# Kernel tuning notes

Measured on AMD Instinct MI355X. Metric: run time of the kernel, lower is better.

Reference implementation:

```python
import jax, jax.numpy as jnp
import numpy as np

DIM = 2048
INTER = 1408
N_EXPERTS = 16
TOP_K = 2
N_SHARED = 2
SHARED_INTER = N_SHARED * INTER  # 2816


def setup_inputs() -> dict:
    key = jax.random.key(0)
    ks = jax.random.split(key, 9)
    s = 0.02
    return {
        "x": jax.random.normal(ks[0], (4, 2048, DIM), dtype=jnp.float32),
        "gate_w": jax.random.normal(ks[1], (N_EXPERTS, DIM), dtype=jnp.float32) * s,
        "w1": jax.random.normal(ks[2], (N_EXPERTS, INTER, DIM), dtype=jnp.float32) * s,
        "w2": jax.random.normal(ks[3], (N_EXPERTS, DIM, INTER), dtype=jnp.float32) * s,
        "w3": jax.random.normal(ks[4], (N_EXPERTS, INTER, DIM), dtype=jnp.float32) * s,
        "sw1": jax.random.normal(ks[5], (SHARED_INTER, DIM), dtype=jnp.float32) * s,
        "sw2": jax.random.normal(ks[6], (DIM, SHARED_INTER), dtype=jnp.float32) * s,
        "sw3": jax.random.normal(ks[7], (SHARED_INTER, DIM), dtype=jnp.float32) * s,
    }


def _swiglu(t, wa, wb, wo):
    # t: [T, d_in]; wa, wb: [d_h, d_in]; wo: [d_out, d_h]
    h = jax.nn.silu(t @ wa.T) * (t @ wb.T)
    return h @ wo.T


def reference(x, gate_w, w1, w2, w3, sw1, sw2, sw3):
    shape = x.shape
    t = x.reshape(-1, DIM)                      # [T, dim]
    scores = jax.nn.softmax(t @ gate_w.T, axis=-1)  # [T, E]
    weights, indices = jax.lax.top_k(scores, TOP_K)  # [T, k] each

    y = jnp.zeros_like(t)
    # Small fixed loop over experts (structurally distinct weights).
    # Per-token combine weight for expert e: sum over top-k slots routed to e
    # (matches y[idx] += expert(x[idx]) * weights[idx, top]; zero weight for
    # unrouted tokens reproduces the counts[i]==0 skip exactly).
    for e in range(N_EXPERTS):
        w_e = jnp.sum(jnp.where(indices == e, weights, 0.0), axis=-1)  # [T]
        y = y + _swiglu(t, w1[e], w3[e], w2[e]) * w_e[:, None]

    z = _swiglu(t, sw1, sw3, sw2)               # shared experts MLP
    return (y + z).reshape(shape)
```

## Files before the change

### kernel.cpp

```cpp
#include <hip/hip_runtime.h>
#include <hip/hip_bf16.h>

#define DIM 2048
#define INTER 1408
#define NEXP 16
#define NTOK 8192
#define SINTER 2816
#define BM 256
#define BN 128
#define BK 32

typedef __attribute__((ext_vector_type(8))) short bf16x8;
typedef __attribute__((ext_vector_type(4))) float f32x4;
typedef __attribute__((ext_vector_type(8))) unsigned short u16x8;

__device__ __forceinline__ unsigned short f2bf(float f) {
    union { float f; unsigned u; } a; a.f = f;
    unsigned r = a.u + 0x7fffu + ((a.u >> 16) & 1u);
    return (unsigned short)(r >> 16);
}

__device__ __forceinline__ void gload16(const void* g, void* lds) {
    __builtin_amdgcn_global_load_lds(
        (const __attribute__((address_space(1))) void*)g,
        (__attribute__((address_space(3))) void*)lds, 16, 0, 0);
}

__device__ __forceinline__ void stage_f32(const float* g, unsigned short* ldsdst) {
    float4 a = *(const float4*)g;
    float4 b = *(const float4*)(g + 4);
    u16x8 o = { f2bf(a.x), f2bf(a.y), f2bf(a.z), f2bf(a.w),
                f2bf(b.x), f2bf(b.y), f2bf(b.z), f2bf(b.w) };
    *(u16x8*)ldsdst = o;
}

__global__ __launch_bounds__(256) void cast_bf16(const float* __restrict__ s,
                                                 unsigned short* __restrict__ d,
                                                 long long n) {
    long long i = ((long long)blockIdx.x * 256 + threadIdx.x) * 8;
    if (i >= n) return;
    float4 a = *(const float4*)(s + i), b = *(const float4*)(s + i + 4);
    u16x8 o = { f2bf(a.x), f2bf(a.y), f2bf(a.z), f2bf(a.w),
                f2bf(b.x), f2bf(b.y), f2bf(b.z), f2bf(b.w) };
    *(u16x8*)(d + i) = o;
}

__global__ __launch_bounds__(256) void gate_topk(
    const float* __restrict__ x, const float* __restrict__ gw,
    int* __restrict__ counts, int* __restrict__ toklist, float* __restrict__ tokw) {
    int wave = threadIdx.x >> 6;
    int lane = threadIdx.x & 63;
    int tok  = blockIdx.x * 4 + wave;
    const float* xr = x + (size_t)tok * DIM;

    float part[NEXP];
#pragma unroll
    for (int e = 0; e < NEXP; ++e) part[e] = 0.f;
#pragma unroll
    for (int c = 0; c < DIM / 256; ++c) {
        float4 xv = *(const float4*)(xr + c * 256 + lane * 4);
#pragma unroll
        for (int e = 0; e < NEXP; ++e) {
            float4 g = *(const float4*)(gw + e * DIM + c * 256 + lane * 4);
            part[e] += xv.x * g.x + xv.y * g.y + xv.z * g.z + xv.w * g.w;
        }
    }
#pragma unroll
    for (int e = 0; e < NEXP; ++e) {
        float v = part[e];
#pragma unroll
        for (int off = 32; off; off >>= 1) v += __shfl_xor(v, off);
        part[e] = v;
    }
    float mx = part[0];
#pragma unroll
    for (int e = 1; e < NEXP; ++e) mx = fmaxf(mx, part[e]);
    float Z = 0.f;
#pragma unroll
    for (int e = 0; e < NEXP; ++e) Z += expf(part[e] - mx);
    int i1 = 0; float m1 = part[0];
#pragma unroll
    for (int e = 1; e < NEXP; ++e) if (part[e] > m1) { m1 = part[e]; i1 = e; }
    int i2 = -1; float m2 = -1e30f;
#pragma unroll
    for (int e = 0; e < NEXP; ++e) if (e != i1 && part[e] > m2) { m2 = part[e]; i2 = e; }
    if (lane == 0) {
        float w1v = expf(m1 - mx) / Z;
        float w2v = expf(m2 - mx) / Z;
        int p1 = atomicAdd(&counts[i1], 1);
        toklist[i1 * NTOK + p1] = tok; tokw[i1 * NTOK + p1] = w1v;
        int p2 = atomicAdd(&counts[i2], 1);
        toklist[i2 * NTOK + p2] = tok; tokw[i2 * NTOK + p2] = w2v;
    }
}

__global__ void prefix_k(const int* __restrict__ counts, int* __restrict__ base) {
    if (threadIdx.x == 0) {
        int acc = 0;
        for (int e = 0; e < NEXP; ++e) { base[e] = acc; acc += counts[e]; }
        base[16] = acc;
        base[17] = acc + NTOK;
    }
}

template<bool XBF, bool WBF>
__global__ __launch_bounds__(512) void gemm1(
    const float* __restrict__ xf, const unsigned short* __restrict__ xb,
    const float* __restrict__ w1f, const float* __restrict__ w3f,
    const float* __restrict__ sw1f, const float* __restrict__ sw3f,
    const unsigned short* __restrict__ w1b, const unsigned short* __restrict__ w3b,
    const unsigned short* __restrict__ sw1b, const unsigned short* __restrict__ sw3b,
    const int* __restrict__ counts, const int* __restrict__ base,
    const int* __restrict__ toklist, unsigned short* __restrict__ hbuf) {
    const int e   = blockIdx.z;
    const int cnt = (e < NEXP) ? counts[e] : NTOK;
    const int m0  = blockIdx.y * BM;
    if (m0 >= cnt) return;
    const int n0  = blockIdx.x * BN;
    const size_t woff = (size_t)((e < NEXP) ? e : e - NEXP) * INTER * DIM;
    const int hbase = base[e];
    const int* tl = toklist + e * NTOK;

    __shared__ __attribute__((aligned(16))) unsigned short As[BM * BK];
    __shared__ __attribute__((aligned(16))) unsigned short B1s[BN * BK];
    __shared__ __attribute__((aligned(16))) unsigned short B3s[BN * BK];

    const int tid = threadIdx.x;
    const int w = tid >> 6, l = tid & 63;
    const int srow = l >> 2;
    const int scol = (l & 3) * 8;

    int tokA[2];
#pragma unroll
    for (int j = 0; j < 2; ++j) {
        int row  = 32 * w + 16 * j + srow;
        int grow = m0 + row;
        int t;
        if (e >= NEXP) t = grow;
        else t = (grow < cnt) ? tl[grow] : 0;
        tokA[j] = t;
    }
    const int brow = n0 + 16 * w + srow;

    const unsigned short *gA0 = nullptr, *gA1 = nullptr, *gB1 = nullptr, *gB3 = nullptr;
    const float *gA0f = nullptr, *gA1f = nullptr, *gB1f = nullptr, *gB3f = nullptr;
    if constexpr (XBF) {
        gA0 = xb + (size_t)tokA[0] * DIM + scol;
        gA1 = xb + (size_t)tokA[1] * DIM + scol;
    } else {
        gA0f = xf + (size_t)tokA[0] * DIM + scol;
        gA1f = xf + (size_t)tokA[1] * DIM + scol;
    }
    if constexpr (WBF) {
        const unsigned short* b1 = ((e < NEXP) ? w1b : sw1b) + woff;
        const unsigned short* b3 = ((e < NEXP) ? w3b : sw3b) + woff;
        gB1 = b1 + (size_t)brow * DIM + scol;
        gB3 = b3 + (size_t)brow * DIM + scol;
    } else {
        const float* b1 = ((e < NEXP) ? w1f : sw1f) + woff;
        const float* b3 = ((e < NEXP) ? w3f : sw3f) + woff;
        gB1f = b1 + (size_t)brow * DIM + scol;
        gB3f = b3 + (size_t)brow * DIM + scol;
    }

    unsigned short* dA0 = As  + (size_t)(2 * w)     * 512;
    unsigned short* dA1 = As  + (size_t)(2 * w + 1) * 512;
    unsigned short* dB1 = B1s + (size_t)w * 512;
    unsigned short* dB3 = B3s + (size_t)w * 512;

    f32x4 acc1[4][4], acc3[4][4];
#pragma unroll
    for (int m = 0; m < 4; ++m)
#pragma unroll
        for (int n = 0; n < 4; ++n) {
            acc1[m][n] = (f32x4){0.f, 0.f, 0.f, 0.f};
            acc3[m][n] = (f32x4){0.f, 0.f, 0.f, 0.f};
        }

    const int wr = w >> 1, wc = w & 1;
    const int lr = l & 15, lk = (l >> 4) * 8;

    for (int k0 = 0; k0 < DIM; k0 += BK) {
        if constexpr (XBF) {
            gload16(gA0 + k0, dA0);
            gload16(gA1 + k0, dA1);
        } else {
            stage_f32(gA0f + k0, dA0 + l * 8);
            stage_f32(gA1f + k0, dA1 + l * 8);
        }
        if constexpr (WBF) {
            gload16(gB1 + k0, dB1);
            gload16(gB3 + k0, dB3);
        } else {
            stage_f32(gB1f + k0, dB1 + l * 8);
            stage_f32(gB3f + k0, dB3 + l * 8);
        }
        __syncthreads();
        bf16x8 af[4], b1q[4], b3q[4];
#pragma unroll
        for (int m = 0; m < 4; ++m)
            af[m] = *(const bf16x8*)(As + (wr * 64 + m * 16 + lr) * BK + lk);
#pragma unroll
        for (int n = 0; n < 4; ++n) {
            b1q[n] = *(const bf16x8*)(B1s + (wc * 64 + n * 16 + lr) * BK + lk);
            b3q[n] = *(const bf16x8*)(B3s + (wc * 64 + n * 16 + lr) * BK + lk);
        }
#pragma unroll
        for (int m = 0; m < 4; ++m)
#pragma unroll
            for (int n = 0; n < 4; ++n) {
                acc1[m][n] = __builtin_amdgcn_mfma_f32_16x16x32_bf16(af[m], b1q[n], acc1[m][n], 0, 0, 0);
                acc3[m][n] = __builtin_amdgcn_mfma_f32_16x16x32_bf16(af[m], b3q[n], acc3[m][n], 0, 0, 0);
            }
        __syncthreads();
    }
#pragma unroll
    for (int m = 0; m < 4; ++m) {
#pragma unroll
        for (int i = 0; i < 4; ++i) {
            int row  = wr * 64 + m * 16 + (l >> 4) * 4 + i;
            int grow = m0 + row;
            if (grow < cnt) {
                size_t ro = (size_t)(hbase + grow) * INTER;
#pragma unroll
                for (int n = 0; n < 4; ++n) {
                    int col = n0 + wc * 64 + n * 16 + lr;
                    float a = acc1[m][n][i];
                    float h = a / (1.f + __expf(-a)) * acc3[m][n][i];
                    hbuf[ro + col] = f2bf(h);
                }
            }
        }
    }
}

template<bool WBF>
__global__ __launch_bounds__(512) void gemm2(
    const unsigned short* __restrict__ hbuf,
    const float* __restrict__ w2f, const float* __restrict__ sw2f,
    const unsigned short* __restrict__ w2b, const unsigned short* __restrict__ sw2b,
    const int* __restrict__ counts, const int* __restrict__ base,
    const int* __restrict__ toklist, const float* __restrict__ tokw,
    float* __restrict__ out) {
    const int e   = blockIdx.z;
    const int cnt = (e < NEXP) ? counts[e] : NTOK;
    const int m0  = blockIdx.y * BM;
    if (m0 >= cnt) return;
    const int n0  = blockIdx.x * BN;
    const int hbase = base[e];
    const size_t bstride = (e < NEXP) ? INTER : SINTER;

    const unsigned short* Bb = nullptr; const float* Bf = nullptr;
    if constexpr (WBF)
        Bb = (e < NEXP) ? w2b + (size_t)e * DIM * INTER : sw2b + (size_t)(e - NEXP) * INTER;
    else
        Bf = (e < NEXP) ? w2f + (size_t)e * DIM * INTER : sw2f + (size_t)(e - NEXP) * INTER;

    __shared__ __attribute__((aligned(16))) unsigned short As[BM * BK];
    __shared__ __attribute__((aligned(16))) unsigned short Bs[BN * BK];

    const int tid = threadIdx.x;
    const int w = tid >> 6, l = tid & 63;
    const int srow = l >> 2;
    const int scol = (l & 3) * 8;

    const unsigned short* gA0 = hbuf + (size_t)(hbase + m0 + 32 * w + srow) * INTER + scol;
    const unsigned short* gA1 = hbuf + (size_t)(hbase + m0 + 32 * w + 16 + srow) * INTER + scol;
    const int brow = n0 + 16 * w + srow;
    const unsigned short* gB = nullptr; const float* gBf = nullptr;
    if constexpr (WBF) gB  = Bb + (size_t)brow * bstride + scol;
    else               gBf = Bf + (size_t)brow * bstride + scol;

    unsigned short* dA0 = As + (size_t)(2 * w)     * 512;
    unsigned short* dA1 = As + (size_t)(2 * w + 1) * 512;
    unsigned short* dB  = Bs + (size_t)w * 512;

    f32x4 acc[4][4];
#pragma unroll
    for (int m = 0; m < 4; ++m)
#pragma unroll
        for (int n = 0; n < 4; ++n) acc[m][n] = (f32x4){0.f, 0.f, 0.f, 0.f};

    const int wr = w >> 1, wc = w & 1;
    const int lr = l & 15, lk = (l >> 4) * 8;

    for (int k0 = 0; k0 < INTER; k0 += BK) {
        gload16(gA0 + k0, dA0);
        gload16(gA1 + k0, dA1);
        if constexpr (WBF) gload16(gB + k0, dB);
        else               stage_f32(gBf + k0, dB + l * 8);
        __syncthreads();
        bf16x8 af[4], bq[4];
#pragma unroll
        for (int m = 0; m < 4; ++m)
            af[m] = *(const bf16x8*)(As + (wr * 64 + m * 16 + lr) * BK + lk);
#pragma unroll
        for (int n = 0; n < 4; ++n)
            bq[n] = *(const bf16x8*)(Bs + (wc * 64 + n * 16 + lr) * BK + lk);
#pragma unroll
        for (int m = 0; m < 4; ++m)
#pragma unroll
            for (int n = 0; n < 4; ++n)
                acc[m][n] = __builtin_amdgcn_mfma_f32_16x16x32_bf16(af[m], bq[n], acc[m][n], 0, 0, 0);
        __syncthreads();
    }
#pragma unroll
    for (int m = 0; m < 4; ++m) {
#pragma unroll
        for (int i = 0; i < 4; ++i) {
            int row  = wr * 64 + m * 16 + (l >> 4) * 4 + i;
            int grow = m0 + row;
            if (grow < cnt) {
                int tok; float wt;
                if (e < NEXP) { tok = toklist[e * NTOK + grow]; wt = tokw[e * NTOK + grow]; }
                else          { tok = grow; wt = 1.f; }
                float* orow = out + (size_t)tok * DIM + n0 + wc * 64 + lr;
#pragma unroll
                for (int n = 0; n < 4; ++n)
                    unsafeAtomicAdd(orow + n * 16, acc[m][n][i] * wt);
            }
        }
    }
}

extern "C" void kernel_launch(void* const* d_in, const int* in_sizes, int n_in,
                              void* d_out, int out_size, void* d_ws, size_t ws_size,
                              hipStream_t stream) {
    const float* x   = (const float*)d_in[0];
    const float* gw  = (const float*)d_in[1];
    const float* w1  = (const float*)d_in[2];
    const float* w2  = (const float*)d_in[3];
    const float* w3  = (const float*)d_in[4];
    const float* sw1 = (const float*)d_in[5];
    const float* sw2 = (const float*)d_in[6];
    const float* sw3 = (const float*)d_in[7];
    float* out = (float*)d_out;

    char* ws = (char*)d_ws;
    int*   counts  = (int*)ws;
    int*   basep   = (int*)(ws + 128);
    int*   toklist = (int*)(ws + 4096);
    float* tokw    = (float*)(ws + 4096 + (size_t)NEXP * NTOK * 4);
    unsigned short* hbuf = (unsigned short*)(ws + (2u << 20));

    const size_t hbytes = (size_t)4 * NTOK * INTER * 2;
    const size_t offx   = (2ull << 20) + hbytes;
    const size_t xbytes = (size_t)NTOK * DIM * 2;
    const size_t offw   = offx + xbytes;
    const size_t wB     = (size_t)NEXP * INTER * DIM * 2;
    const size_t swB    = (size_t)SINTER * DIM * 2;
    const size_t tier2_end = offw + 3 * wB + 3 * swB;

    int tier = (ws_size >= tier2_end) ? 2 : (ws_size >= offw ? 1 : 0);

    unsigned short* xb   = (unsigned short*)(ws + offx);
    unsigned short* w1b  = (unsigned short*)(ws + offw);
    unsigned short* w3b  = (unsigned short*)(ws + offw + wB);
    unsigned short* w2b  = (unsigned short*)(ws + offw + 2 * wB);
    unsigned short* sw1b = (unsigned short*)(ws + offw + 3 * wB);
    unsigned short* sw3b = (unsigned short*)(ws + offw + 3 * wB + swB);
    unsigned short* sw2b = (unsigned short*)(ws + offw + 3 * wB + 2 * swB);

    hipMemsetAsync(counts, 0, 64, stream);
    hipMemsetAsync(d_out, 0, (size_t)out_size * sizeof(float), stream);

    gate_topk<<<NTOK / 4, 256, 0, stream>>>(x, gw, counts, toklist, tokw);
    prefix_k<<<1, 64, 0, stream>>>(counts, basep);

    auto cast = [&](const float* s, unsigned short* d, long long n) {
        cast_bf16<<<(int)((n / 8 + 255) / 256), 256, 0, stream>>>(s, d, n);
    };
    if (tier >= 1) cast(x, xb, (long long)NTOK * DIM);
    if (tier == 2) {
        cast(w1, w1b, (long long)NEXP * INTER * DIM);
        cast(w3, w3b, (long long)NEXP * INTER * DIM);
        cast(w2, w2b, (long long)NEXP * INTER * DIM);
        cast(sw1, sw1b, (long long)SINTER * DIM);
        cast(sw3, sw3b, (long long)SINTER * DIM);
        cast(sw2, sw2b, (long long)SINTER * DIM);
    }

    dim3 g1(INTER / BN, NTOK / BM, 18);
    dim3 g2(DIM / BN, NTOK / BM, 18);
    if (tier == 2) {
        gemm1<true, true><<<g1, 512, 0, stream>>>(x, xb, w1, w3, sw1, sw3,
            w1b, w3b, sw1b, sw3b, counts, basep, toklist, hbuf);
        gemm2<true><<<g2, 512, 0, stream>>>(hbuf, w2, sw2, w2b, sw2b,
            counts, basep, toklist, tokw, out);
    } else if (tier == 1) {
        gemm1<true, false><<<g1, 512, 0, stream>>>(x, xb, w1, w3, sw1, sw3,
            w1b, w3b, sw1b, sw3b, counts, basep, toklist, hbuf);
        gemm2<false><<<g2, 512, 0, stream>>>(hbuf, w2, sw2, w2b, sw2b,
            counts, basep, toklist, tokw, out);
    } else {
        gemm1<false, false><<<g1, 512, 0, stream>>>(x, xb, w1, w3, sw1, sw3,
            w1b, w3b, sw1b, sw3b, counts, basep, toklist, hbuf);
        gemm2<false><<<g2, 512, 0, stream>>>(hbuf, w2, sw2, w2b, sw2b,
            counts, basep, toklist, tokw, out);
    }
}
```

Baseline: 1.443 ms.

## Add 4-stage LDS prefetch pipeline with swizzled layout and larger gemm2 tile

Both GEMMs now keep four LDS stages and prefetch three K-steps ahead, using explicit vmcnt waits and s_barrier in place of a full __syncthreads after each load. The LDS tiles use an XOR swizzle to reduce bank conflicts, MFMA sections run at raised wave priority, and gemm2's N tile doubles to 256 with each warp covering 8x4 fragments. The fp32 fallback tiers are removed, so the workspace is assumed large enough for the bf16 weight copies. The aim is to hide global-load latency and sync stalls, at the cost of much more LDS (occupancy is capped at two blocks) and more registers in gemm2.

```diff
diff --git a/kernel.cpp b/kernel.cpp
--- a/kernel.cpp
+++ b/kernel.cpp
@@ -6,9 +6,6 @@
 #define NEXP 16
 #define NTOK 8192
 #define SINTER 2816
-#define BM 256
-#define BN 128
-#define BK 32
 
 typedef __attribute__((ext_vector_type(8))) short bf16x8;
 typedef __attribute__((ext_vector_type(4))) float f32x4;
@@ -24,14 +21,6 @@
     __builtin_amdgcn_global_load_lds(
         (const __attribute__((address_space(1))) void*)g,
         (__attribute__((address_space(3))) void*)lds, 16, 0, 0);
-}
-
-__device__ __forceinline__ void stage_f32(const float* g, unsigned short* ldsdst) {
-    float4 a = *(const float4*)g;
-    float4 b = *(const float4*)(g + 4);
-    u16x8 o = { f2bf(a.x), f2bf(a.y), f2bf(a.z), f2bf(a.w),
-                f2bf(b.x), f2bf(b.y), f2bf(b.z), f2bf(b.w) };
-    *(u16x8*)ldsdst = o;
 }
 
 __global__ __launch_bounds__(256) void cast_bf16(const float* __restrict__ s,
@@ -103,70 +92,56 @@
     }
 }
 
-template<bool XBF, bool WBF>
-__global__ __launch_bounds__(512) void gemm1(
-    const float* __restrict__ xf, const unsigned short* __restrict__ xb,
-    const float* __restrict__ w1f, const float* __restrict__ w3f,
-    const float* __restrict__ sw1f, const float* __restrict__ sw3f,
+__device__ __forceinline__ int swz(int r) { return (r ^ (r >> 2)) & 3; }
+
+__global__ __launch_bounds__(512, 2) void gemm1(
+    const unsigned short* __restrict__ xb,
     const unsigned short* __restrict__ w1b, const unsigned short* __restrict__ w3b,
     const unsigned short* __restrict__ sw1b, const unsigned short* __restrict__ sw3b,
     const int* __restrict__ counts, const int* __restrict__ base,
     const int* __restrict__ toklist, unsigned short* __restrict__ hbuf) {
     const int e   = blockIdx.z;
     const int cnt = (e < NEXP) ? counts[e] : NTOK;
-    const int m0  = blockIdx.y * BM;
+    const int m0  = blockIdx.y * 256;
     if (m0 >= cnt) return;
-    const int n0  = blockIdx.x * BN;
+    const int n0  = blockIdx.x * 128;
     const size_t woff = (size_t)((e < NEXP) ? e : e - NEXP) * INTER * DIM;
+    const unsigned short* B1 = ((e < NEXP) ? w1b : sw1b) + woff;
+    const unsigned short* B3 = ((e < NEXP) ? w3b : sw3b) + woff;
     const int hbase = base[e];
     const int* tl = toklist + e * NTOK;
 
-    __shared__ __attribute__((aligned(16))) unsigned short As[BM * BK];
-    __shared__ __attribute__((aligned(16))) unsigned short B1s[BN * BK];
-    __shared__ __attribute__((aligned(16))) unsigned short B3s[BN * BK];
+    __shared__ __attribute__((aligned(16))) unsigned short As[4][8192];
+    __shared__ __attribute__((aligned(16))) unsigned short B1s[4][4096];
+    __shared__ __attribute__((aligned(16))) unsigned short B3s[4][4096];
 
     const int tid = threadIdx.x;
     const int w = tid >> 6, l = tid & 63;
-    const int srow = l >> 2;
-    const int scol = (l & 3) * 8;
-
-    int tokA[2];
-#pragma unroll
-    for (int j = 0; j < 2; ++j) {
-        int row  = 32 * w + 16 * j + srow;
-        int grow = m0 + row;
-        int t;
-        if (e >= NEXP) t = grow;
-        else t = (grow < cnt) ? tl[grow] : 0;
-        tokA[j] = t;
-    }
-    const int brow = n0 + 16 * w + srow;
-
-    const unsigned short *gA0 = nullptr, *gA1 = nullptr, *gB1 = nullptr, *gB3 = nullptr;
-    const float *gA0f = nullptr, *gA1f = nullptr, *gB1f = nullptr, *gB3f = nullptr;
-    if constexpr (XBF) {
-        gA0 = xb + (size_t)tokA[0] * DIM + scol;
-        gA1 = xb + (size_t)tokA[1] * DIM + scol;
-    } else {
-        gA0f = xf + (size_t)tokA[0] * DIM + scol;
-        gA1f = xf + (size_t)tokA[1] * DIM + scol;
-    }
-    if constexpr (WBF) {
-        const unsigned short* b1 = ((e < NEXP) ? w1b : sw1b) + woff;
-        const unsigned short* b3 = ((e < NEXP) ? w3b : sw3b) + woff;
-        gB1 = b1 + (size_t)brow * DIM + scol;
-        gB3 = b3 + (size_t)brow * DIM + scol;
-    } else {
-        const float* b1 = ((e < NEXP) ? w1f : sw1f) + woff;
-        const float* b3 = ((e < NEXP) ? w3f : sw3f) + woff;
-        gB1f = b1 + (size_t)brow * DIM + scol;
-        gB3f = b3 + (size_t)brow * DIM + scol;
-    }
-
-    unsigned short* dA0 = As  + (size_t)(2 * w)     * 512;
-    unsigned short* dA1 = As  + (size_t)(2 * w + 1) * 512;
-    unsigned short* dB1 = B1s + (size_t)w * 512;
-    unsigned short* dB3 = B3s + (size_t)w * 512;
+    const int wr = w >> 1, wc = w & 1;
+    const int lr = l & 15, hi = l >> 4;
+
+    const int row0 = tid >> 2, row1 = row0 + 128;
+    const int c0 = (tid & 3) ^ swz(row0);
+    int g0 = m0 + row0, g1 = m0 + row1;
+    int t0, t1;
+    if (e < NEXP) { t0 = (g0 < cnt) ? tl[g0] : 0; t1 = (g1 < cnt) ? tl[g1] : 0; }
+    else          { t0 = g0; t1 = g1; }
+    const unsigned short* aSrc0 = xb + (size_t)t0 * DIM + c0 * 8;
+    const unsigned short* aSrc1 = xb + (size_t)t1 * DIM + c0 * 8;
+    const unsigned short* b1Src = B1 + (size_t)(n0 + row0) * DIM + c0 * 8;
+    const unsigned short* b3Src = B3 + (size_t)(n0 + row0) * DIM + c0 * 8;
+
+    int aoff[4], boff[4];
+#pragma unroll
+    for (int m = 0; m < 4; ++m) {
+        int r = wr * 64 + m * 16 + lr;
+        aoff[m] = r * 64 + ((swz(r) ^ hi) << 4);
+    }
+#pragma unroll
+    for (int n = 0; n < 4; ++n) {
+        int r = wc * 64 + n * 16 + lr;
+        boff[n] = r * 64 + ((swz(r) ^ hi) << 4);
+    }
 
     f32x4 acc1[4][4], acc3[4][4];
 #pragma unroll
@@ -177,48 +152,60 @@
             acc3[m][n] = (f32x4){0.f, 0.f, 0.f, 0.f};
         }
 
-    const int wr = w >> 1, wc = w & 1;
-    const int lr = l & 15, lk = (l >> 4) * 8;
-
-    for (int k0 = 0; k0 < DIM; k0 += BK) {
-        if constexpr (XBF) {
-            gload16(gA0 + k0, dA0);
-            gload16(gA1 + k0, dA1);
-        } else {
-            stage_f32(gA0f + k0, dA0 + l * 8);
-            stage_f32(gA1f + k0, dA1 + l * 8);
-        }
-        if constexpr (WBF) {
-            gload16(gB1 + k0, dB1);
-            gload16(gB3 + k0, dB3);
-        } else {
-            stage_f32(gB1f + k0, dB1 + l * 8);
-            stage_f32(gB3f + k0, dB3 + l * 8);
-        }
-        __syncthreads();
-        bf16x8 af[4], b1q[4], b3q[4];
+    const int H = DIM / 32;
+
+    auto STAGE = [&](int hh) {
+        int hb = hh & 3;
+        int kc = hh * 32;
+        gload16(aSrc0 + kc, &As[hb][tid * 8]);
+        gload16(aSrc1 + kc, &As[hb][4096 + tid * 8]);
+        gload16(b1Src + kc, &B1s[hb][tid * 8]);
+        gload16(b3Src + kc, &B3s[hb][tid * 8]);
+    };
+
+    STAGE(0); STAGE(1); STAGE(2);
+    asm volatile("s_waitcnt vmcnt(8)" ::: "memory");
+    __builtin_amdgcn_s_barrier();
+
+    for (int h = 0; h < H; ++h) {
+        const int hb = h & 3;
+        bf16x8 af[4], b1f[4], b3f[4];
 #pragma unroll
         for (int m = 0; m < 4; ++m)
-            af[m] = *(const bf16x8*)(As + (wr * 64 + m * 16 + lr) * BK + lk);
+            af[m] = *(const bf16x8*)((const char*)&As[hb][0] + aoff[m]);
 #pragma unroll
         for (int n = 0; n < 4; ++n) {
-            b1q[n] = *(const bf16x8*)(B1s + (wc * 64 + n * 16 + lr) * BK + lk);
-            b3q[n] = *(const bf16x8*)(B3s + (wc * 64 + n * 16 + lr) * BK + lk);
-        }
+            b1f[n] = *(const bf16x8*)((const char*)&B1s[hb][0] + boff[n]);
+            b3f[n] = *(const bf16x8*)((const char*)&B3s[hb][0] + boff[n]);
+        }
+        if (h + 3 < H) {
+            STAGE(h + 3);
+            asm volatile("s_waitcnt vmcnt(8)" ::: "memory");
+        } else if (h == H - 3) {
+            asm volatile("s_waitcnt vmcnt(4)" ::: "memory");
+        } else if (h == H - 2) {
+            asm volatile("s_waitcnt vmcnt(0)" ::: "memory");
+        }
+        __builtin_amdgcn_s_barrier();
+        asm volatile("s_waitcnt lgkmcnt(0)" ::: "memory");
+        __builtin_amdgcn_sched_barrier(0);
+        __builtin_amdgcn_s_setprio(1);
 #pragma unroll
         for (int m = 0; m < 4; ++m)
 #pragma unroll
             for (int n = 0; n < 4; ++n) {
-                acc1[m][n] = __builtin_amdgcn_mfma_f32_16x16x32_bf16(af[m], b1q[n], acc1[m][n], 0, 0, 0);
-                acc3[m][n] = __builtin_amdgcn_mfma_f32_16x16x32_bf16(af[m], b3q[n], acc3[m][n], 0, 0, 0);
+                acc1[m][n] = __builtin_amdgcn_mfma_f32_16x16x32_bf16(af[m], b1f[n], acc1[m][n], 0, 0, 0);
+                acc3[m][n] = __builtin_amdgcn_mfma_f32_16x16x32_bf16(af[m], b3f[n], acc3[m][n], 0, 0, 0);
             }
-        __syncthreads();
-    }
+        __builtin_amdgcn_s_setprio(0);
+        __builtin_amdgcn_s_barrier();
+    }
+
 #pragma unroll
     for (int m = 0; m < 4; ++m) {
 #pragma unroll
         for (int i = 0; i < 4; ++i) {
-            int row  = wr * 64 + m * 16 + (l >> 4) * 4 + i;
+            int row  = wr * 64 + m * 16 + hi * 4 + i;
             int grow = m0 + row;
             if (grow < cnt) {
                 size_t ro = (size_t)(hbase + grow) * INTER;
@@ -226,89 +213,113 @@
                 for (int n = 0; n < 4; ++n) {
                     int col = n0 + wc * 64 + n * 16 + lr;
                     float a = acc1[m][n][i];
-                    float h = a / (1.f + __expf(-a)) * acc3[m][n][i];
-                    hbuf[ro + col] = f2bf(h);
+                    float hv = a / (1.f + __expf(-a)) * acc3[m][n][i];
+                    hbuf[ro + col] = f2bf(hv);
                 }
             }
         }
     }
 }
 
-template<bool WBF>
-__global__ __launch_bounds__(512) void gemm2(
+__global__ __launch_bounds__(512, 2) void gemm2(
     const unsigned short* __restrict__ hbuf,
-    const float* __restrict__ w2f, const float* __restrict__ sw2f,
     const unsigned short* __restrict__ w2b, const unsigned short* __restrict__ sw2b,
     const int* __restrict__ counts, const int* __restrict__ base,
     const int* __restrict__ toklist, const float* __restrict__ tokw,
     float* __restrict__ out) {
     const int e   = blockIdx.z;
     const int cnt = (e < NEXP) ? counts[e] : NTOK;
-    const int m0  = blockIdx.y * BM;
+    const int m0  = blockIdx.y * 256;
     if (m0 >= cnt) return;
-    const int n0  = blockIdx.x * BN;
+    const int n0  = blockIdx.x * 256;
     const int hbase = base[e];
     const size_t bstride = (e < NEXP) ? INTER : SINTER;
-
-    const unsigned short* Bb = nullptr; const float* Bf = nullptr;
-    if constexpr (WBF)
-        Bb = (e < NEXP) ? w2b + (size_t)e * DIM * INTER : sw2b + (size_t)(e - NEXP) * INTER;
-    else
-        Bf = (e < NEXP) ? w2f + (size_t)e * DIM * INTER : sw2f + (size_t)(e - NEXP) * INTER;
-
-    __shared__ __attribute__((aligned(16))) unsigned short As[BM * BK];
-    __shared__ __attribute__((aligned(16))) unsigned short Bs[BN * BK];
+    const unsigned short* Bb = (e < NEXP) ? w2b + (size_t)e * DIM * INTER
+                                          : sw2b + (size_t)(e - NEXP) * INTER;
+
+    __shared__ __attribute__((aligned(16))) unsigned short Ah[4][8192];
+    __shared__ __attribute__((aligned(16))) unsigned short Bh[4][8192];
 
     const int tid = threadIdx.x;
     const int w = tid >> 6, l = tid & 63;
-    const int srow = l >> 2;
-    const int scol = (l & 3) * 8;
-
-    const unsigned short* gA0 = hbuf + (size_t)(hbase + m0 + 32 * w + srow) * INTER + scol;
-    const unsigned short* gA1 = hbuf + (size_t)(hbase + m0 + 32 * w + 16 + srow) * INTER + scol;
-    const int brow = n0 + 16 * w + srow;
-    const unsigned short* gB = nullptr; const float* gBf = nullptr;
-    if constexpr (WBF) gB  = Bb + (size_t)brow * bstride + scol;
-    else               gBf = Bf + (size_t)brow * bstride + scol;
-
-    unsigned short* dA0 = As + (size_t)(2 * w)     * 512;
-    unsigned short* dA1 = As + (size_t)(2 * w + 1) * 512;
-    unsigned short* dB  = Bs + (size_t)w * 512;
-
-    f32x4 acc[4][4];
-#pragma unroll
-    for (int m = 0; m < 4; ++m)
+    const int wr = w >> 2, wc = w & 3;
+    const int lr = l & 15, hi = l >> 4;
+
+    const int row0 = tid >> 2, row1 = row0 + 128;
+    const int c0 = (tid & 3) ^ swz(row0);
+    const unsigned short* aSrc0 = hbuf + (size_t)(hbase + m0 + row0) * INTER + c0 * 8;
+    const unsigned short* aSrc1 = hbuf + (size_t)(hbase + m0 + row1) * INTER + c0 * 8;
+    const unsigned short* bSrc0 = Bb + (size_t)(n0 + row0) * bstride + c0 * 8;
+    const unsigned short* bSrc1 = Bb + (size_t)(n0 + row1) * bstride + c0 * 8;
+
+    int aoff[8], boff[4];
+#pragma unroll
+    for (int m = 0; m < 8; ++m) {
+        int r = wr * 128 + m * 16 + lr;
+        aoff[m] = r * 64 + ((swz(r) ^ hi) << 4);
+    }
+#pragma unroll
+    for (int n = 0; n < 4; ++n) {
+        int r = wc * 64 + n * 16 + lr;
+        boff[n] = r * 64 + ((swz(r) ^ hi) << 4);
+    }
+
+    f32x4 acc[8][4];
+#pragma unroll
+    for (int m = 0; m < 8; ++m)
 #pragma unroll
         for (int n = 0; n < 4; ++n) acc[m][n] = (f32x4){0.f, 0.f, 0.f, 0.f};
 
-    const int wr = w >> 1, wc = w & 1;
-    const int lr = l & 15, lk = (l >> 4) * 8;
-
-    for (int k0 = 0; k0 < INTER; k0 += BK) {
-        gload16(gA0 + k0, dA0);
-        gload16(gA1 + k0, dA1);
-        if constexpr (WBF) gload16(gB + k0, dB);
-        else               stage_f32(gBf + k0, dB + l * 8);
-        __syncthreads();
-        bf16x8 af[4], bq[4];
-#pragma unroll
-        for (int m = 0; m < 4; ++m)
-            af[m] = *(const bf16x8*)(As + (wr * 64 + m * 16 + lr) * BK + lk);
+    const int H = INTER / 32;
+
+    auto STAGE = [&](int hh) {
+        int hb = hh & 3;
+        int kc = hh * 32;
+        gload16(aSrc0 + kc, &Ah[hb][tid * 8]);
+        gload16(aSrc1 + kc, &Ah[hb][4096 + tid * 8]);
+        gload16(bSrc0 + kc, &Bh[hb][tid * 8]);
+        gload16(bSrc1 + kc, &Bh[hb][4096 + tid * 8]);
+    };
+
+    STAGE(0); STAGE(1); STAGE(2);
+    asm volatile("s_waitcnt vmcnt(8)" ::: "memory");
+    __builtin_amdgcn_s_barrier();
+
+    for (int h = 0; h < H; ++h) {
+        const int hb = h & 3;
+        bf16x8 af[8], bf[4];
+#pragma unroll
+        for (int m = 0; m < 8; ++m)
+            af[m] = *(const bf16x8*)((const char*)&Ah[hb][0] + aoff[m]);
 #pragma unroll
         for (int n = 0; n < 4; ++n)
-            bq[n] = *(const bf16x8*)(Bs + (wc * 64 + n * 16 + lr) * BK + lk);
-#pragma unroll
-        for (int m = 0; m < 4; ++m)
+            bf[n] = *(const bf16x8*)((const char*)&Bh[hb][0] + boff[n]);
+        if (h + 3 < H) {
+            STAGE(h + 3);
+            asm volatile("s_waitcnt vmcnt(8)" ::: "memory");
+        } else if (h == H - 3) {
+            asm volatile("s_waitcnt vmcnt(4)" ::: "memory");
+        } else if (h == H - 2) {
+            asm volatile("s_waitcnt vmcnt(0)" ::: "memory");
+        }
+        __builtin_amdgcn_s_barrier();
+        asm volatile("s_waitcnt lgkmcnt(0)" ::: "memory");
+        __builtin_amdgcn_sched_barrier(0);
+        __builtin_amdgcn_s_setprio(1);
+#pragma unroll
+        for (int m = 0; m < 8; ++m)
 #pragma unroll
             for (int n = 0; n < 4; ++n)
-                acc[m][n] = __builtin_amdgcn_mfma_f32_16x16x32_bf16(af[m], bq[n], acc[m][n], 0, 0, 0);
-        __syncthreads();
-    }
-#pragma unroll
-    for (int m = 0; m < 4; ++m) {
+                acc[m][n] = __builtin_amdgcn_mfma_f32_16x16x32_bf16(af[m], bf[n], acc[m][n], 0, 0, 0);
+        __builtin_amdgcn_s_setprio(0);
+        __builtin_amdgcn_s_barrier();
+    }
+
+#pragma unroll
+    for (int m = 0; m < 8; ++m) {
 #pragma unroll
         for (int i = 0; i < 4; ++i) {
-            int row  = wr * 64 + m * 16 + (l >> 4) * 4 + i;
+            int row  = wr * 128 + m * 16 + hi * 4 + i;
             int grow = m0 + row;
             if (grow < cnt) {
                 int tok; float wt;
@@ -349,9 +360,6 @@
     const size_t offw   = offx + xbytes;
     const size_t wB     = (size_t)NEXP * INTER * DIM * 2;
     const size_t swB    = (size_t)SINTER * DIM * 2;
-    const size_t tier2_end = offw + 3 * wB + 3 * swB;
-
-    int tier = (ws_size >= tier2_end) ? 2 : (ws_size >= offw ? 1 : 0);
 
     unsigned short* xb   = (unsigned short*)(ws + offx);
     unsigned short* w1b  = (unsigned short*)(ws + offw);
@@ -370,32 +378,16 @@
     auto cast = [&](const float* s, unsigned short* d, long long n) {
         cast_bf16<<<(int)((n / 8 + 255) / 256), 256, 0, stream>>>(s, d, n);
     };
-    if (tier >= 1) cast(x, xb, (long long)NTOK * DIM);
-    if (tier == 2) {
-        cast(w1, w1b, (long long)NEXP * INTER * DIM);
-        cast(w3, w3b, (long long)NEXP * INTER * DIM);
-        cast(w2, w2b, (long long)NEXP * INTER * DIM);
-        cast(sw1, sw1b, (long long)SINTER * DIM);
-        cast(sw3, sw3b, (long long)SINTER * DIM);
-        cast(sw2, sw2b, (long long)SINTER * DIM);
-    }
-
-    dim3 g1(INTER / BN, NTOK / BM, 18);
-    dim3 g2(DIM / BN, NTOK / BM, 18);
-    if (tier == 2) {
-        gemm1<true, true><<<g1, 512, 0, stream>>>(x, xb, w1, w3, sw1, sw3,
-            w1b, w3b, sw1b, sw3b, counts, basep, toklist, hbuf);
-        gemm2<true><<<g2, 512, 0, stream>>>(hbuf, w2, sw2, w2b, sw2b,
-            counts, basep, toklist, tokw, out);
-    } else if (tier == 1) {
-        gemm1<true, false><<<g1, 512, 0, stream>>>(x, xb, w1, w3, sw1, sw3,
-            w1b, w3b, sw1b, sw3b, counts, basep, toklist, hbuf);
-        gemm2<false><<<g2, 512, 0, stream>>>(hbuf, w2, sw2, w2b, sw2b,
-            counts, basep, toklist, tokw, out);
-    } else {
-        gemm1<false, false><<<g1, 512, 0, stream>>>(x, xb, w1, w3, sw1, sw3,
-            w1b, w3b, sw1b, sw3b, counts, basep, toklist, hbuf);
-        gemm2<false><<<g2, 512, 0, stream>>>(hbuf, w2, sw2, w2b, sw2b,
-            counts, basep, toklist, tokw, out);
-    }
-}
+    cast(x, xb, (long long)NTOK * DIM);
+    cast(w1, w1b, (long long)NEXP * INTER * DIM);
+    cast(w3, w3b, (long long)NEXP * INTER * DIM);
+    cast(w2, w2b, (long long)NEXP * INTER * DIM);
+    cast(sw1, sw1b, (long long)SINTER * DIM);
+    cast(sw3, sw3b, (long long)SINTER * DIM);
+    cast(sw2, sw2b, (long long)SINTER * DIM);
+
+    gemm1<<<dim3(INTER / 128, NTOK / 256, 18), 512, 0, stream>>>(
+        xb, w1b, w3b, sw1b, sw3b, counts, basep, toklist, hbuf);
+    gemm2<<<dim3(DIM / 256, NTOK / 256, 18), 512, 0, stream>>>(
+        hbuf, w2b, sw2b, counts, basep, toklist, tokw, out);
+}
```

New measurement: 1.352 ms. 6.3% less time.
